# Kernel tuning notes

Measured on AMD Instinct MI355X. Metric: run time of the kernel, lower is better.

Reference implementation:

```python
import jax, jax.numpy as jnp
import numpy as np

B, T, V, H = 32, 512, 1024, 256

def setup_inputs() -> dict:
    key = jax.random.key(0)
    k = jax.random.split(key, 6)
    glorot_x = (6.0 / (V + H)) ** 0.5
    glorot_h = (6.0 / (H + H)) ** 0.5
    glorot_d = (6.0 / (H + V)) ** 0.5
    return {
        "X": jax.random.normal(k[0], (B, T, V), dtype=jnp.float32),
        "Wx": jax.random.uniform(k[1], (V, H), jnp.float32, -glorot_x, glorot_x),
        "Wh": jax.random.uniform(k[2], (H, H), jnp.float32, -glorot_h, glorot_h),
        "b": jnp.zeros((H,), jnp.float32),
        "Wd": jax.random.uniform(k[3], (H, V), jnp.float32, -glorot_d, glorot_d),
        "bd": jnp.zeros((V,), jnp.float32),
    }

def reference(X, Wx, Wh, b, Wd, bd):
    # Precompute input projections for all timesteps: [T, B, H]
    xproj = jnp.einsum('btv,vh->tbh', X, Wx) + b
    h0 = jnp.zeros((X.shape[0], Wh.shape[0]), X.dtype)

    def step(h, xp):
        h_new = jnp.tanh(xp + h @ Wh)  # SimpleRNNCell: tanh(Wx x + Wh h + b)
        return h_new, h_new

    new_state, Ys = jax.lax.scan(step, h0, xproj)  # Ys: [T, B, H]
    Y = jnp.transpose(Ys, (1, 0, 2)).reshape(-1, Wh.shape[0])  # [B*T, H]
    out = jax.nn.softmax(Y @ Wd + bd, axis=-1)  # [B*T, V]
    return out, new_state
```

## Files before the change

kernel.cpp:

```cpp
#include <hip/hip_runtime.h>

typedef float f32x4 __attribute__((ext_vector_type(4)));
typedef _Float16 f16x8 __attribute__((ext_vector_type(8)));
typedef _Float16 f16x4 __attribute__((ext_vector_type(4)));

__device__ __forceinline__ float tanh_fast(float x) {
  float e = __builtin_amdgcn_exp2f(x * 2.885390081777927f);
  return 1.0f - 2.0f * __builtin_amdgcn_rcpf(e + 1.0f);
}

__global__ __launch_bounds__(256) void k_transpose_cast(
    const float* __restrict__ in, _Float16* __restrict__ outp, int R, int C)
{
  __shared__ float tile[32][33];
  const int tx = threadIdx.x & 31, ty = threadIdx.x >> 5;
  const int tc = blockIdx.x * 32, tr = blockIdx.y * 32;
#pragma unroll
  for (int i = 0; i < 32; i += 8)
    tile[ty + i][tx] = in[(size_t)(tr + ty + i) * C + tc + tx];
  __syncthreads();
#pragma unroll
  for (int i = 0; i < 32; i += 8)
    outp[(size_t)(tc + ty + i) * R + tr + tx] = (_Float16)tile[tx][ty + i];
}

__global__ __launch_bounds__(256) void k_transpose_cast_perm(
    const float* __restrict__ in, _Float16* __restrict__ outp, int R, int C)
{
  __shared__ float tile[32][33];
  const int tx = threadIdx.x & 31, ty = threadIdx.x >> 5;
  const int tc = blockIdx.x * 32, tr = blockIdx.y * 32;
#pragma unroll
  for (int i = 0; i < 32; i += 8)
    tile[ty + i][tx] = in[(size_t)(tr + ty + i) * C + tc + tx];
  __syncthreads();
  const int r = tr + tx;
  const int p = (r & ~63) | ((r & 15) << 2) | ((r >> 4) & 3);
#pragma unroll
  for (int i = 0; i < 32; i += 8)
    outp[(size_t)(tc + ty + i) * R + p] = (_Float16)tile[tx][ty + i];
}

__global__ __launch_bounds__(256) void k_gemm1(
    const float* __restrict__ X, const _Float16* __restrict__ WxT,
    const float* __restrict__ bias, float* __restrict__ xp_packed)
{
  __shared__ _Float16 As[64][72];
  __shared__ _Float16 Bs[256][72];
  const int tid = threadIdx.x;
  const int lane = tid & 63, w = tid >> 6;
  const int l15 = lane & 15, lq = lane >> 4;
  const int m0 = blockIdx.x * 64;

  f32x4 acc[16];
#pragma unroll
  for (int i = 0; i < 16; ++i) acc[i] = (f32x4){0.f, 0.f, 0.f, 0.f};

  for (int kc = 0; kc < 16; ++kc) {
    const int k0 = kc * 64;
#pragma unroll
    for (int it = 0; it < 4; ++it) {
      int q = tid + it * 256;
      int r = q >> 4, k4 = (q & 15) * 4;
      f32x4 v = *(const f32x4*)(X + (size_t)(m0 + r) * 1024 + k0 + k4);
      f16x4 hv;
      hv[0] = (_Float16)v[0]; hv[1] = (_Float16)v[1];
      hv[2] = (_Float16)v[2]; hv[3] = (_Float16)v[3];
      *(f16x4*)(&As[r][k4]) = hv;
    }
#pragma unroll
    for (int it = 0; it < 8; ++it) {
      int q = tid + it * 256;
      int n = q >> 3, k8 = (q & 7) * 8;
      *(f16x8*)(&Bs[n][k8]) = *(const f16x8*)(WxT + (size_t)n * 1024 + k0 + k8);
    }
    __syncthreads();
    f16x8 a[2];
#pragma unroll
    for (int ks = 0; ks < 2; ++ks)
      a[ks] = *(const f16x8*)(&As[w * 16 + l15][ks * 32 + lq * 8]);
#pragma unroll
    for (int ct = 0; ct < 16; ++ct) {
#pragma unroll
      for (int ks = 0; ks < 2; ++ks) {
        f16x8 bfr = *(const f16x8*)(&Bs[ct * 16 + l15][ks * 32 + lq * 8]);
        acc[ct] = __builtin_amdgcn_mfma_f32_16x16x32_f16(a[ks], bfr, acc[ct], 0, 0, 0);
      }
    }
    __syncthreads();
  }
#pragma unroll
  for (int ct = 0; ct < 16; ++ct) {
    int ncol = ct * 16 + l15;
    float bvv = bias[ncol];
    int w_s = ncol >> 6, j_s = (ncol >> 4) & 3, i_s = ncol & 15;
#pragma unroll
    for (int r = 0; r < 4; ++r) {
      int m = m0 + w * 16 + lq * 4 + r;
      int tt = m & 511, bb = m >> 9;
      int g_s = bb >> 2, lq_s = bb & 3;
      size_t idx = ((((size_t)tt * 8 + g_s) * 4 + w_s) * 64 + (lq_s * 16 + i_s)) * 4 + j_s;
      xp_packed[idx] = acc[ct][r] + bvv;
    }
  }
}

__global__ __launch_bounds__(256, 1) void k_scan(
    const float* __restrict__ xp_packed,
    const _Float16* __restrict__ WhTp,
    _Float16* __restrict__ Yt,
    float* __restrict__ hT)
{
  __shared__ char hbuf[2][4224];
  const int tid = threadIdx.x;
  const int lane = tid & 63, w = tid >> 6;
  const int l15 = lane & 15, lq = lane >> 4;
  const int g = blockIdx.x;

  for (int i = tid; i < 2112; i += 256) ((float*)hbuf)[i] = 0.f;

  f16x8 bf[4][8];
#pragma unroll
  for (int j = 0; j < 4; ++j)
#pragma unroll
    for (int i = 0; i < 8; ++i) {
      int ks = (2 * w + i) & 7;
      bf[j][i] = *(const f16x8*)(WhTp + (w * 64 + j * 16 + l15) * 256 + ks * 32 + lq * 8);
    }

  char* hz = (char*)&hbuf[0][0];
  const int rd_base = (l15 & 3) * 1056 + w * 128 + lq * 16;
  const int wr_base = lq * 1056 + w * 128 + l15 * 8;
  const bool m1 = (lq & 1) != 0, m2 = (lq & 2) != 0;

  const float* xpb = xp_packed + (((size_t)g * 4 + w) * 64 + lane) * 4;
  _Float16* yb = Yt + ((size_t)(g * 4 + lq)) * 256 + w * 64 + l15 * 4;
  float* hTb = hT + (g * 4 + lq) * 256 + w * 64 + l15;

  __syncthreads();

  f32x4 x0 = *(const f32x4*)(xpb);
  f32x4 x1 = *(const f32x4*)(xpb + 8192);

#define SCAN_STEP(T, CUR, X, LAST)                                             \
  {                                                                            \
    const int t = (T);                                                         \
    f16x8 af[8];                                                               \
       \
    af[0] = *(const f16x8*)(hz + rd_base + (CUR) * 4224 + 0 * 64);             \
    af[1] = *(const f16x8*)(hz + rd_base + (CUR) * 4224 + 1 * 64);             \
    asm volatile("" ::: "memory");                                             \
    __builtin_amdgcn_s_barrier();                                              \
    asm volatile("" ::: "memory");                                             \
    _Pragma("unroll")                                                          \
    for (int i = 2; i < 8; ++i)                                                \
      af[i] = *(const f16x8*)(hz + rd_base + (CUR) * 4224 + i * 64);           \
    f32x4 xcur = X;                                                            \
    f32x4 aca[4], acb[4];                                                      \
    _Pragma("unroll")                                                          \
    for (int j = 0; j < 4; ++j) {                                              \
      f32x4 zz = {0.f, 0.f, 0.f, 0.f};                                         \
      f32x4 xi;                                                                \
      xi[0] = xcur[j]; xi[1] = xcur[j]; xi[2] = xcur[j]; xi[3] = xcur[j];      \
      aca[j] = __builtin_amdgcn_mfma_f32_16x16x32_f16(af[0], bf[j][0], xi, 0, 0, 0); \
      acb[j] = __builtin_amdgcn_mfma_f32_16x16x32_f16(af[4], bf[j][4], zz, 0, 0, 0); \
    }                                                                          \
    {                                                    \
      int tn = t + 2; if (tn > 511) tn = 511;                                  \
      X = *(const f32x4*)(xpb + (size_t)tn * 8192);                            \
    }                                                                          \
    _Pragma("unroll")                                                          \
    for (int i = 1; i < 4; ++i) {                                              \
      _Pragma("unroll")                                                        \
      for (int j = 0; j < 4; ++j) {                                            \
        aca[j] = __builtin_amdgcn_mfma_f32_16x16x32_f16(af[i], bf[j][i], aca[j], 0, 0, 0); \
        acb[j] = __builtin_amdgcn_mfma_f32_16x16x32_f16(af[i + 4], bf[j][i + 4], acb[j], 0, 0, 0); \
      }                                                                        \
    }                                                                          \
    f16x4 h4;                                                                  \
    float vv[4];                                                               \
    _Pragma("unroll")                                                          \
    for (int j = 0; j < 4; ++j) {                                              \
      f32x4 s = aca[j] + acb[j];                                               \
      float t0 = m1 ? s[1] : s[0];                                             \
      float t1 = m1 ? s[3] : s[2];                                             \
      float v = tanh_fast(m2 ? t1 : t0);                                       \
      vv[j] = v;                                                               \
      h4[j] = (_Float16)v;                                                     \
    }                                                                          \
    *(f16x4*)(hz + wr_base + ((CUR) ^ 1) * 4224) = h4;                         \
    *(f16x4*)(hz + wr_base + ((CUR) ^ 1) * 4224 + 512) = h4;                   \
    *(f16x4*)(yb + (size_t)t * 8192) = h4;                                     \
    if (LAST) {                                                                \
      _Pragma("unroll")                                                        \
      for (int j = 0; j < 4; ++j) hTb[j * 16] = vv[j];                         \
    }                                                                          \
    asm volatile("s_waitcnt lgkmcnt(0)" ::: "memory");                         \
  }

  SCAN_STEP(0, 0, x0, 0)
  for (int tp = 0; tp < 255; ++tp) {
    SCAN_STEP(2 * tp + 1, 1, x1, 0)
    SCAN_STEP(2 * tp + 2, 0, x0, 0)
  }
  SCAN_STEP(511, 1, x1, 1)
#undef SCAN_STEP
}

__global__ __launch_bounds__(512) void k_gemm3(
    const _Float16* __restrict__ Yt,
    const _Float16* __restrict__ WdTp,
    const float* __restrict__ bd,
    float* __restrict__ out)
{
  __shared__ _Float16 As[16][264];
  __shared__ _Float16 Bs[128][264];
  __shared__ _Float16 lg[16][1040];
  const int tid = threadIdx.x;
  const int lane = tid & 63, w = tid >> 6;
  const int l15 = lane & 15, lq = lane >> 4;
  const int m0 = blockIdx.x * 16;
  const int b = m0 >> 9, t0 = m0 & 511;

  {
    int r = tid >> 5, k8 = (tid & 31) * 8;
    *(f16x8*)(&As[r][k8]) = *(const f16x8*)(Yt + ((size_t)(t0 + r) * 32 + b) * 256 + k8);
  }
  __syncthreads();
  f16x8 a[8];
#pragma unroll
  for (int ks = 0; ks < 8; ++ks)
    a[ks] = *(const f16x8*)(&As[l15][ks * 32 + lq * 8]);

  for (int cc = 0; cc < 8; ++cc) {
    const int c0 = cc * 128;
    __syncthreads();
#pragma unroll
    for (int i = 0; i < 8; ++i) {
      int q = i * 512 + tid;
      int n = q >> 5, k8 = (q & 31) * 8;
      *(f16x8*)(&Bs[n][k8]) = *(const f16x8*)(WdTp + (size_t)(c0 + n) * 256 + k8);
    }
    __syncthreads();
    int ncol = c0 + w * 16 + l15;
    f32x4 acc = {0.f, 0.f, 0.f, 0.f};
#pragma unroll
    for (int ks = 0; ks < 8; ++ks) {
      f16x8 bfr = *(const f16x8*)(&Bs[w * 16 + l15][ks * 32 + lq * 8]);
      acc = __builtin_amdgcn_mfma_f32_16x16x32_f16(a[ks], bfr, acc, 0, 0, 0);
    }
    float bvv = bd[ncol];
#pragma unroll
    for (int r = 0; r < 4; ++r)
      lg[lq * 4 + r][ncol] = (_Float16)(acc[r] + bvv);
  }
  __syncthreads();

  const int row = tid >> 5, j = tid & 31;
  float mx = -1e30f;
#pragma unroll
  for (int k = 0; k < 32; ++k)
    mx = fmaxf(mx, (float)lg[row][j + k * 32]);
#pragma unroll
  for (int m = 1; m < 32; m <<= 1)
    mx = fmaxf(mx, __shfl_xor(mx, m, 64));
  float s = 0.f;
#pragma unroll
  for (int k = 0; k < 32; ++k)
    s += __builtin_amdgcn_exp2f(((float)lg[row][j + k * 32] - mx) * 1.44269504088896f);
#pragma unroll
  for (int m = 1; m < 32; m <<= 1)
    s += __shfl_xor(s, m, 64);
  const float rinv = __builtin_amdgcn_rcpf(s);
  float* orow = out + (size_t)(m0 + row) * 1024;
#pragma unroll
  for (int k = 0; k < 8; ++k) {
    int c = k * 128 + j * 4;
    f32x4 vv;
#pragma unroll
    for (int u = 0; u < 4; ++u)
      vv[u] = __builtin_amdgcn_exp2f(((float)lg[row][c + u] - mx) * 1.44269504088896f) * rinv;
    *(f32x4*)(orow + c) = vv;
  }
}

extern "C" void kernel_launch(void* const* d_in, const int* in_sizes, int n_in,
                              void* d_out, int out_size, void* d_ws, size_t ws_size,
                              hipStream_t stream) {
  const float* X  = (const float*)d_in[0];
  const float* Wx = (const float*)d_in[1];
  const float* Wh = (const float*)d_in[2];
  const float* bv = (const float*)d_in[3];
  const float* Wd = (const float*)d_in[4];
  const float* bd = (const float*)d_in[5];
  float* out = (float*)d_out;

  char* ws = (char*)d_ws;
  float*    xp_packed = (float*)(ws);
  _Float16* Yt    = (_Float16*)(ws + (16u << 20));
  _Float16* WxT   = (_Float16*)(ws + (24u << 20));
  _Float16* WhTp  = (_Float16*)(ws + (24u << 20) + (512u << 10));
  _Float16* WdTp  = (_Float16*)(ws + (24u << 20) + (640u << 10));

  k_transpose_cast<<<dim3(8, 32), 256, 0, stream>>>(Wx, WxT, 1024, 256);
  k_transpose_cast_perm<<<dim3(8, 8),  256, 0, stream>>>(Wh, WhTp, 256, 256);
  k_transpose_cast_perm<<<dim3(32, 8), 256, 0, stream>>>(Wd, WdTp, 256, 1024);
  k_gemm1<<<dim3(256), 256, 0, stream>>>(X, WxT, bv, xp_packed);
  k_scan<<<dim3(8), 256, 0, stream>>>(xp_packed, WhTp, Yt, out + 16384 * 1024);
  k_gemm3<<<dim3(1024), 512, 0, stream>>>(Yt, WdTp, bd, out);
}
```

Measured before the change: 376.3 us.

## Split recurrent scan across eight waves with shorter MFMA dependency chains

```diff
diff --git a/kernel.cpp b/kernel.cpp
--- a/kernel.cpp
+++ b/kernel.cpp
@@ -1,8 +1,10 @@
 #include <hip/hip_runtime.h>
 
 typedef float f32x4 __attribute__((ext_vector_type(4)));
+typedef float f32x2 __attribute__((ext_vector_type(2)));
 typedef _Float16 f16x8 __attribute__((ext_vector_type(8)));
 typedef _Float16 f16x4 __attribute__((ext_vector_type(4)));
+typedef _Float16 f16x2 __attribute__((ext_vector_type(2)));
 
 __device__ __forceinline__ float tanh_fast(float x) {
   float e = __builtin_amdgcn_exp2f(x * 2.885390081777927f);
@@ -35,7 +37,7 @@
     tile[ty + i][tx] = in[(size_t)(tr + ty + i) * C + tc + tx];
   __syncthreads();
   const int r = tr + tx;
-  const int p = (r & ~63) | ((r & 15) << 2) | ((r >> 4) & 3);
+  const int p = (r & ~31) | ((r & 15) << 1) | ((r >> 4) & 1);
 #pragma unroll
   for (int i = 0; i < 32; i += 8)
     outp[(size_t)(tc + ty + i) * R + p] = (_Float16)tile[tx][ty + i];
@@ -93,19 +95,19 @@
   for (int ct = 0; ct < 16; ++ct) {
     int ncol = ct * 16 + l15;
     float bvv = bias[ncol];
-    int w_s = ncol >> 6, j_s = (ncol >> 4) & 3, i_s = ncol & 15;
+    int w_s = ncol >> 5, j_s = (ncol >> 4) & 1, i_s = ncol & 15;
 #pragma unroll
     for (int r = 0; r < 4; ++r) {
       int m = m0 + w * 16 + lq * 4 + r;
       int tt = m & 511, bb = m >> 9;
       int g_s = bb >> 2, lq_s = bb & 3;
-      size_t idx = ((((size_t)tt * 8 + g_s) * 4 + w_s) * 64 + (lq_s * 16 + i_s)) * 4 + j_s;
+      size_t idx = (((size_t)tt * 8 + g_s) * 8 + w_s) * 128 + (lq_s * 16 + i_s) * 2 + j_s;
       xp_packed[idx] = acc[ct][r] + bvv;
     }
   }
 }
 
-__global__ __launch_bounds__(256, 1) void k_scan(
+__global__ __launch_bounds__(512, 2) void k_scan(
     const float* __restrict__ xp_packed,
     const _Float16* __restrict__ WhTp,
     _Float16* __restrict__ Yt,
@@ -117,83 +119,82 @@
   const int l15 = lane & 15, lq = lane >> 4;
   const int g = blockIdx.x;
 
-  for (int i = tid; i < 2112; i += 256) ((float*)hbuf)[i] = 0.f;
-
-  f16x8 bf[4][8];
-#pragma unroll
-  for (int j = 0; j < 4; ++j)
+  for (int i = tid; i < 2112; i += 512) ((float*)hbuf)[i] = 0.f;
+
+  f16x8 bf[2][8];
+#pragma unroll
+  for (int j = 0; j < 2; ++j)
 #pragma unroll
     for (int i = 0; i < 8; ++i) {
-      int ks = (2 * w + i) & 7;
-      bf[j][i] = *(const f16x8*)(WhTp + (w * 64 + j * 16 + l15) * 256 + ks * 32 + lq * 8);
+      int ks = (w + i) & 7;
+      bf[j][i] = *(const f16x8*)(WhTp + (w * 32 + j * 16 + l15) * 256 + ks * 32 + lq * 8);
     }
 
   char* hz = (char*)&hbuf[0][0];
-  const int rd_base = (l15 & 3) * 1056 + w * 128 + lq * 16;
-  const int wr_base = lq * 1056 + w * 128 + l15 * 8;
+  const int rd_base = (l15 & 3) * 1056 + w * 64 + lq * 16;
+  const int wr_base = lq * 1056 + w * 64 + l15 * 4;
   const bool m1 = (lq & 1) != 0, m2 = (lq & 2) != 0;
 
-  const float* xpb = xp_packed + (((size_t)g * 4 + w) * 64 + lane) * 4;
-  _Float16* yb = Yt + ((size_t)(g * 4 + lq)) * 256 + w * 64 + l15 * 4;
-  float* hTb = hT + (g * 4 + lq) * 256 + w * 64 + l15;
-
-  __syncthreads();
-
-  f32x4 x0 = *(const f32x4*)(xpb);
-  f32x4 x1 = *(const f32x4*)(xpb + 8192);
+  const float* xpb = xp_packed + ((size_t)g * 8 + w) * 128 + lane * 2;
+  _Float16* yb = Yt + ((size_t)(g * 4 + lq)) * 256 + w * 32 + l15 * 2;
+  float* hTb = hT + (g * 4 + lq) * 256 + w * 32 + l15;
+
+  __syncthreads();
+
+  f32x2 x0 = *(const f32x2*)(xpb);
+  f32x2 x1 = *(const f32x2*)(xpb + 8192);
 
 #define SCAN_STEP(T, CUR, X, LAST)                                             \
   {                                                                            \
     const int t = (T);                                                         \
     f16x8 af[8];                                                               \
-       \
+               \
     af[0] = *(const f16x8*)(hz + rd_base + (CUR) * 4224 + 0 * 64);             \
-    af[1] = *(const f16x8*)(hz + rd_base + (CUR) * 4224 + 1 * 64);             \
     asm volatile("" ::: "memory");                                             \
     __builtin_amdgcn_s_barrier();                                              \
     asm volatile("" ::: "memory");                                             \
     _Pragma("unroll")                                                          \
-    for (int i = 2; i < 8; ++i)                                                \
+    for (int i = 1; i < 8; ++i)                                                \
       af[i] = *(const f16x8*)(hz + rd_base + (CUR) * 4224 + i * 64);           \
-    f32x4 xcur = X;                                                            \
-    f32x4 aca[4], acb[4];                                                      \
+    f32x2 xcur = X;                                                            \
+    f32x4 acc[2][4];                                                           \
     _Pragma("unroll")                                                          \
-    for (int j = 0; j < 4; ++j) {                                              \
-      f32x4 zz = {0.f, 0.f, 0.f, 0.f};                                         \
-      f32x4 xi;                                                                \
-      xi[0] = xcur[j]; xi[1] = xcur[j]; xi[2] = xcur[j]; xi[3] = xcur[j];      \
-      aca[j] = __builtin_amdgcn_mfma_f32_16x16x32_f16(af[0], bf[j][0], xi, 0, 0, 0); \
-      acb[j] = __builtin_amdgcn_mfma_f32_16x16x32_f16(af[4], bf[j][4], zz, 0, 0, 0); \
+    for (int j = 0; j < 2; ++j) {                                              \
+      _Pragma("unroll")                                                        \
+      for (int c = 0; c < 4; ++c) {                                            \
+        f32x4 zz = {0.f, 0.f, 0.f, 0.f};                                       \
+        acc[j][c] = __builtin_amdgcn_mfma_f32_16x16x32_f16(af[2 * c], bf[j][2 * c], zz, 0, 0, 0); \
+      }                                                                        \
     }                                                                          \
     {                                                    \
       int tn = t + 2; if (tn > 511) tn = 511;                                  \
-      X = *(const f32x4*)(xpb + (size_t)tn * 8192);                            \
+      X = *(const f32x2*)(xpb + (size_t)tn * 8192);                            \
     }                                                                          \
     _Pragma("unroll")                                                          \
-    for (int i = 1; i < 4; ++i) {                                              \
+    for (int j = 0; j < 2; ++j) {                                              \
       _Pragma("unroll")                                                        \
-      for (int j = 0; j < 4; ++j) {                                            \
-        aca[j] = __builtin_amdgcn_mfma_f32_16x16x32_f16(af[i], bf[j][i], aca[j], 0, 0, 0); \
-        acb[j] = __builtin_amdgcn_mfma_f32_16x16x32_f16(af[i + 4], bf[j][i + 4], acb[j], 0, 0, 0); \
-      }                                                                        \
-    }                                                                          \
-    f16x4 h4;                                                                  \
-    float vv[4];                                                               \
+      for (int c = 0; c < 4; ++c)                                              \
+        acc[j][c] = __builtin_amdgcn_mfma_f32_16x16x32_f16(af[2 * c + 1], bf[j][2 * c + 1], acc[j][c], 0, 0, 0); \
+    }                                                                          \
+    f16x2 h2;                                                                  \
+    float vv[2];                                                               \
     _Pragma("unroll")                                                          \
-    for (int j = 0; j < 4; ++j) {                                              \
-      f32x4 s = aca[j] + acb[j];                                               \
+    for (int j = 0; j < 2; ++j) {                                              \
+      f32x4 s01 = acc[j][0] + acc[j][1];                                       \
+      f32x4 s23 = acc[j][2] + acc[j][3];                                       \
+      f32x4 s = s01 + s23;                                                     \
       float t0 = m1 ? s[1] : s[0];                                             \
       float t1 = m1 ? s[3] : s[2];                                             \
-      float v = tanh_fast(m2 ? t1 : t0);                                       \
+      float v = tanh_fast((m2 ? t1 : t0) + xcur[j]);                           \
       vv[j] = v;                                                               \
-      h4[j] = (_Float16)v;                                                     \
-    }                                                                          \
-    *(f16x4*)(hz + wr_base + ((CUR) ^ 1) * 4224) = h4;                         \
-    *(f16x4*)(hz + wr_base + ((CUR) ^ 1) * 4224 + 512) = h4;                   \
-    *(f16x4*)(yb + (size_t)t * 8192) = h4;                                     \
+      h2[j] = (_Float16)v;                                                     \
+    }                                                                          \
+    *(f16x2*)(hz + wr_base + ((CUR) ^ 1) * 4224) = h2;                         \
+    *(f16x2*)(hz + wr_base + ((CUR) ^ 1) * 4224 + 512) = h2;                   \
+    *(f16x2*)(yb + (size_t)t * 8192) = h2;                                     \
     if (LAST) {                                                                \
-      _Pragma("unroll")                                                        \
-      for (int j = 0; j < 4; ++j) hTb[j * 16] = vv[j];                         \
+      hTb[0] = vv[0];                                                          \
+      hTb[16] = vv[1];                                                         \
     }                                                                          \
     asm volatile("s_waitcnt lgkmcnt(0)" ::: "memory");                         \
   }
@@ -306,6 +307,6 @@
   k_transpose_cast_perm<<<dim3(8, 8),  256, 0, stream>>>(Wh, WhTp, 256, 256);
   k_transpose_cast_perm<<<dim3(32, 8), 256, 0, stream>>>(Wd, WdTp, 256, 1024);
   k_gemm1<<<dim3(256), 256, 0, stream>>>(X, WxT, bv, xp_packed);
-  k_scan<<<dim3(8), 256, 0, stream>>>(xp_packed, WhTp, Yt, out + 16384 * 1024);
+  k_scan<<<dim3(8), 512, 0, stream>>>(xp_packed, WhTp, Yt, out + 16384 * 1024);
   k_gemm3<<<dim3(1024), 512, 0, stream>>>(Yt, WdTp, bd, out);
 }
```

Result: faster. 338.8 us (-10.0%).
